# Kernel tuning notes

Hardware: AMD Instinct MI355X
Metric: run time of the kernel (lower is better)

## Reference

```python
import jax, jax.numpy as jnp
import numpy as np

SCALE = 1.0  # noise std used in the Gaussian log-pdf
HIGH = jax.lax.Precision.HIGHEST


def setup_inputs() -> dict:
    key = jax.random.key(0)
    k1, k2, k3 = jax.random.split(key, 3)
    B, N, D, T = 64, 256, 64, 4096
    data = jax.random.normal(k1, (B, N, D), dtype=jnp.float32)
    targets = jax.random.normal(k2, (B, N), dtype=jnp.float32)
    task_pool = jax.random.normal(k3, (T, D, 1), dtype=jnp.float32)
    return {"data": data, "targets": targets, "task_pool": task_pool}


def reference(data, targets, task_pool):
    # data: [B, N, D], targets: [B, N], task_pool: [T, D, 1]
    W = jnp.squeeze(task_pool).T  # [D, T]
    # Per-point, per-task Gaussian log-likelihood of targets under each task weight.
    Z = jnp.einsum('bnd,dt->bnt', data, W, precision=HIGH)  # [B, N, T]
    resid = targets[:, :, None] - Z
    logp = jax.scipy.stats.norm.logpdf(resid, loc=0.0, scale=SCALE)  # [B, N, T]
    # alpha for step i (i >= 1) is the cumulative log-lik over points 0..i-1.
    cum = jnp.cumsum(logp, axis=1)          # [B, N, T]
    alphas = cum[:, :-1]                    # [B, N-1, T], alphas[:, i-1] = alpha at step i
    post = jax.nn.softmax(alphas, axis=-1)  # posterior over tasks per step
    # MMSE weight per step: posterior-weighted average of task weights.
    w_mmse = jnp.einsum('bit,dt->bid', post, W, precision=HIGH)  # [B, N-1, D]
    preds_rest = jnp.einsum('bid,bid->bi', data[:, 1:], w_mmse)  # [B, N-1]
    # Step 0: prior mean weight (uniform average over task pool).
    pred0 = data[:, 0] @ W.mean(axis=1)  # [B]
    return jnp.concatenate([pred0[:, None], preds_rest], axis=1)  # [B, N]
```

## Files before the change

kernel.cpp:

```cpp
#include <hip/hip_runtime.h>
#include <math.h>

#define BB 64
#define NN 256
#define DD 64
#define TT 4096

#define NCH 16
#define CT (TT/NCH)
#define THREADS 512
#define WAVES 8
#define NB 16
#define NGRP (NN/NB)
#define BN (BB*NN)

#define NHL2E (-0.72134752044448170368f)

typedef __bf16 bf16x8 __attribute__((ext_vector_type(8)));
typedef float  f32x4  __attribute__((ext_vector_type(4)));

#define SHR1 0x111
#define SHR2 0x112
#define SHR4 0x114
#define SHR8 0x118

template<int C>
__device__ __forceinline__ float dppf(float x) {
  return __int_as_float(__builtin_amdgcn_update_dpp(
      0, __float_as_int(x), C, 0xf, 0xf, true));
}

__device__ __forceinline__ float bcast15(float x) {
  return __int_as_float(__builtin_amdgcn_ds_swizzle(__float_as_int(x), 0x1F0));
}

__device__ __forceinline__ unsigned short f2bf(float f) {
  unsigned int u = __float_as_uint(f);
  unsigned int r = u + 0x7FFFu + ((u >> 16) & 1u);
  return (unsigned short)(r >> 16);
}
__device__ __forceinline__ float bf2f(unsigned short h) {
  return __uint_as_float(((unsigned int)h) << 16);
}

#define GLOAD_LDS16(gp, lp_) \
  __builtin_amdgcn_global_load_lds((const __attribute__((address_space(1))) void*)(gp), \
                                   (__attribute__((address_space(3))) void*)(lp_), 16, 0, 0)

union FragU { unsigned int u[4]; bf16x8 v; };

__device__ __forceinline__ void merge8(const float2 (*sb)[16], int lane,
                                       float2* __restrict__ part, size_t obase) {
  const int col = lane & 15;
  float2 p0 = sb[0][col];
  float M = p0.x, S = 1.f, V = p0.y;
  #pragma unroll
  for (int w = 1; w < WAVES; ++w) {
    float2 pw = sb[w][col];
    float mn = fmaxf(M, pw.x);
    float ea = __builtin_amdgcn_exp2f(M - mn);
    float eb = __builtin_amdgcn_exp2f(pw.x - mn);
    S = S * ea + eb;
    V = fmaf(V, ea, pw.y * eb);
    M = mn;
  }
  if (lane < 16) {
    float2 lr;
    lr.x = M + __log2f(S);
    lr.y = V / S;
    part[obase + (size_t)col * NCH] = lr;
  }
}

__global__ __launch_bounds__(THREADS, 4)
void mmse_phase1(const float* __restrict__ data,
                 const float* __restrict__ targets,
                 const float* __restrict__ Wp,
                 float2* __restrict__ part)
{
  const int bx   = blockIdx.x;
  const int b    = bx >> 4;
  const int ch   = bx & 15;
  const int tid  = threadIdx.x;
  const int lane = tid & 63;
  const int wave = tid >> 6;

  __shared__ uint4  dbufq[2][256];
  __shared__ float  tgl[NN];
  __shared__ float2 sbuf[2][WAVES][16];

  unsigned char* dbufc = (unsigned char*)dbufq;

  bf16x8 aH[2][2], aL[2][2];
  {
    const int tb = ch * CT + wave * 32;
    #pragma unroll
    for (int tile = 0; tile < 2; ++tile) {
      #pragma unroll
      for (int s = 0; s < 2; ++s) {
        const int row = tb + tile * 16 + (lane & 15);
        const int kb  = s * 32 + (lane >> 4) * 8;
        const float* wp = Wp + (size_t)row * DD + kb;
        FragU hu, lu;
        #pragma unroll
        for (int jj = 0; jj < 4; ++jj) {
          const float f0 = wp[2 * jj], f1 = wp[2 * jj + 1];
          const unsigned short h0 = f2bf(f0), h1 = f2bf(f1);
          const unsigned short g0 = f2bf(f0 - bf2f(h0)), g1 = f2bf(f1 - bf2f(h1));
          hu.u[jj] = (unsigned int)h0 | ((unsigned int)h1 << 16);
          lu.u[jj] = (unsigned int)g0 | ((unsigned int)g1 << 16);
        }
        aH[tile][s] = hu.v; aL[tile][s] = lu.v;
      }
    }
  }

  if (wave == 0)
    GLOAD_LDS16(targets + (size_t)b * NN + lane * 4, tgl);

  const float* __restrict__ dbase = data + (size_t)b * NN * DD;
  const int sn  = tid >> 5;
  const int sk2 = tid & 31;
  const int sphys = (sn * 128 + sk2 * 4) ^ ((sn & 7) << 4);

  {
    const float2 q = *(const float2*)(dbase + (size_t)sn * DD + sk2 * 2);
    const unsigned short h0 = f2bf(q.x), h1 = f2bf(q.y);
    const unsigned short g0 = f2bf(q.x - bf2f(h0)), g1 = f2bf(q.y - bf2f(h1));
    *(unsigned int*)(dbufc + sphys)        = (unsigned int)h0 | ((unsigned int)h1 << 16);
    *(unsigned int*)(dbufc + 2048 + sphys) = (unsigned int)g0 | ((unsigned int)g1 << 16);
  }
  __syncthreads();

  float c8[8];
  #pragma unroll
  for (int i = 0; i < 8; ++i) c8[i] = 0.f;

  const size_t obase0 = (size_t)(b * NN) * NCH + ch;

  #pragma unroll 1
  for (int g = 0; g < NGRP; ++g) {
    const int buf = g & 1;
    const unsigned char* bp = dbufc + buf * 4096;
    const int ra = ((lane & 15) * 128 + (lane >> 4) * 16) ^ ((lane & 7) << 4);
    bf16x8 bh0 = *(const bf16x8*)(bp + ra);
    bf16x8 bh1 = *(const bf16x8*)(bp + (ra ^ 64));
    bf16x8 bl0 = *(const bf16x8*)(bp + 2048 + ra);
    bf16x8 bl1 = *(const bf16x8*)(bp + 2048 + (ra ^ 64));

    float2 q;
    if (g + 1 < NGRP)
      q = *(const float2*)(dbase + (size_t)((g + 1) * NB + sn) * DD + sk2 * 2);

    if (g > 0 && wave == ((g - 1) & 7))
      merge8(sbuf[(g - 1) & 1], lane, part, obase0 + (size_t)((g - 1) * NB) * NCH);

    f32x4 zz[2];
    zz[0] = (f32x4)(0.f); zz[1] = (f32x4)(0.f);
    zz[0] = __builtin_amdgcn_mfma_f32_16x16x32_bf16(aH[0][0], bh0, zz[0], 0, 0, 0);
    zz[0] = __builtin_amdgcn_mfma_f32_16x16x32_bf16(aH[0][0], bl0, zz[0], 0, 0, 0);
    zz[0] = __builtin_amdgcn_mfma_f32_16x16x32_bf16(aL[0][0], bh0, zz[0], 0, 0, 0);
    zz[0] = __builtin_amdgcn_mfma_f32_16x16x32_bf16(aH[0][1], bh1, zz[0], 0, 0, 0);
    zz[0] = __builtin_amdgcn_mfma_f32_16x16x32_bf16(aH[0][1], bl1, zz[0], 0, 0, 0);
    zz[0] = __builtin_amdgcn_mfma_f32_16x16x32_bf16(aL[0][1], bh1, zz[0], 0, 0, 0);
    zz[1] = __builtin_amdgcn_mfma_f32_16x16x32_bf16(aH[1][0], bh0, zz[1], 0, 0, 0);
    zz[1] = __builtin_amdgcn_mfma_f32_16x16x32_bf16(aH[1][0], bl0, zz[1], 0, 0, 0);
    zz[1] = __builtin_amdgcn_mfma_f32_16x16x32_bf16(aL[1][0], bh0, zz[1], 0, 0, 0);
    zz[1] = __builtin_amdgcn_mfma_f32_16x16x32_bf16(aH[1][1], bh1, zz[1], 0, 0, 0);
    zz[1] = __builtin_amdgcn_mfma_f32_16x16x32_bf16(aH[1][1], bl1, zz[1], 0, 0, 0);
    zz[1] = __builtin_amdgcn_mfma_f32_16x16x32_bf16(aL[1][1], bh1, zz[1], 0, 0, 0);

    const float tgf = tgl[g * 16 + (lane & 15)];

    float alpha[8];
    float mloc = -3.4e38f;
    #pragma unroll
    for (int tile = 0; tile < 2; ++tile) {
      #pragma unroll
      for (int r = 0; r < 4; ++r) {
        const int t8 = tile * 4 + r;
        const float z  = zz[tile][r];
        const float rr = tgf - z;
        const float lp = rr * rr * NHL2E;
        float x = lp;
        x += dppf<SHR1>(x);
        x += dppf<SHR2>(x);
        x += dppf<SHR4>(x);
        x += dppf<SHR8>(x);
        const float tot = bcast15(x);
        const float a_ = c8[t8] + (x - lp);
        alpha[t8] = a_;
        c8[t8] += tot;
        mloc = fmaxf(mloc, a_);
      }
    }
    float m = fmaxf(mloc, __shfl_xor(mloc, 16));
    m = fmaxf(m, __shfl_xor(m, 32));
    float sv = 0.f, vv = 0.f;
    #pragma unroll
    for (int tile = 0; tile < 2; ++tile) {
      #pragma unroll
      for (int r = 0; r < 4; ++r) {
        const float p = __builtin_amdgcn_exp2f(alpha[tile * 4 + r] - m);
        sv += p;
        vv = fmaf(p, zz[tile][r], vv);
      }
    }
    sv += __shfl_xor(sv, 16); sv += __shfl_xor(sv, 32);
    vv += __shfl_xor(vv, 16); vv += __shfl_xor(vv, 32);
    if (lane < 16) {
      float2 lr;
      lr.x = m + __log2f(sv);
      lr.y = vv / sv;
      sbuf[buf][wave][lane] = lr;
    }

    if (g + 1 < NGRP) {
      const unsigned short h0 = f2bf(q.x), h1 = f2bf(q.y);
      const unsigned short g0 = f2bf(q.x - bf2f(h0)), g1 = f2bf(q.y - bf2f(h1));
      unsigned char* wb = dbufc + (buf ^ 1) * 4096;
      *(unsigned int*)(wb + sphys)        = (unsigned int)h0 | ((unsigned int)h1 << 16);
      *(unsigned int*)(wb + 2048 + sphys) = (unsigned int)g0 | ((unsigned int)g1 << 16);
    }
    __syncthreads();
  }

  if (wave == ((NGRP - 1) & 7))
    merge8(sbuf[(NGRP - 1) & 1], lane, part, obase0 + (size_t)((NGRP - 1) * NB) * NCH);
}

__global__ __launch_bounds__(256)
void mmse_phase2(const float* __restrict__ part, float* __restrict__ out)
{
  const int gid  = blockIdx.x * 256 + threadIdx.x;
  const int idx  = gid >> 1;
  const int half = gid & 1;
  const float2* __restrict__ p = (const float2*)part + (size_t)idx * NCH + half * 8;
  float M = -3.4e38f, S = 0.f, V = 0.f;
  #pragma unroll
  for (int c = 0; c < 8; ++c) {
    const float2 q = p[c];
    const float mn = fmaxf(M, q.x);
    const float ea = __builtin_amdgcn_exp2f(M - mn);
    const float eb = __builtin_amdgcn_exp2f(q.x - mn);
    S = fmaf(S, ea, eb);
    V = fmaf(V, ea, q.y * eb);
    M = mn;
  }
  const float m2 = __shfl_xor(M, 1), s2 = __shfl_xor(S, 1), v2 = __shfl_xor(V, 1);
  const float mn = fmaxf(M, m2);
  const float ea = __builtin_amdgcn_exp2f(M - mn);
  const float eb = __builtin_amdgcn_exp2f(m2 - mn);
  S = fmaf(S, ea, s2 * eb);
  V = fmaf(V, ea, v2 * eb);
  if (half == 0) out[idx] = V / S;
}

extern "C" void kernel_launch(void* const* d_in, const int* in_sizes, int n_in,
                              void* d_out, int out_size, void* d_ws, size_t ws_size,
                              hipStream_t stream)
{
  const float* data      = (const float*)d_in[0];
  const float* targets   = (const float*)d_in[1];
  const float* task_pool = (const float*)d_in[2];
  float* out = (float*)d_out;

  float2* part = (float2*)d_ws;

  hipLaunchKernelGGL(mmse_phase1, dim3(BB * NCH), dim3(THREADS), 0, stream,
                     data, targets, task_pool, part);
  hipLaunchKernelGGL(mmse_phase2, dim3(2 * BN / 256), dim3(256), 0, stream,
                     (const float*)part, out);
}
```

Before: 120.3 us.

## Process 32 points per barrier step with vectorized loads and native bf16 conversion

Doubles the points per group from 16 to 32, so each loop iteration handles two 16-point halves between barriers. This halves the number of __syncthreads and merge steps. It also switches the data and weight loads to float4 and uses the hardware __bf16 conversion instead of manual bit rounding. MFMA sections are wrapped in s_setprio. The cost is a larger LDS buffer and more registers per iteration, and merge32 now uses 32 lanes.

```diff
diff --git a/kernel.cpp b/kernel.cpp
--- a/kernel.cpp
+++ b/kernel.cpp
@@ -10,12 +10,13 @@
 #define CT (TT/NCH)
 #define THREADS 512
 #define WAVES 8
-#define NB 16
+#define NB 32
 #define NGRP (NN/NB)
 #define BN (BB*NN)
 
 #define NHL2E (-0.72134752044448170368f)
 
+typedef __bf16 bf16x4 __attribute__((ext_vector_type(4)));
 typedef __bf16 bf16x8 __attribute__((ext_vector_type(8)));
 typedef float  f32x4  __attribute__((ext_vector_type(4)));
 
@@ -34,24 +35,13 @@
   return __int_as_float(__builtin_amdgcn_ds_swizzle(__float_as_int(x), 0x1F0));
 }
 
-__device__ __forceinline__ unsigned short f2bf(float f) {
-  unsigned int u = __float_as_uint(f);
-  unsigned int r = u + 0x7FFFu + ((u >> 16) & 1u);
-  return (unsigned short)(r >> 16);
-}
-__device__ __forceinline__ float bf2f(unsigned short h) {
-  return __uint_as_float(((unsigned int)h) << 16);
-}
-
 #define GLOAD_LDS16(gp, lp_) \
   __builtin_amdgcn_global_load_lds((const __attribute__((address_space(1))) void*)(gp), \
                                    (__attribute__((address_space(3))) void*)(lp_), 16, 0, 0)
 
-union FragU { unsigned int u[4]; bf16x8 v; };
-
-__device__ __forceinline__ void merge8(const float2 (*sb)[16], int lane,
-                                       float2* __restrict__ part, size_t obase) {
-  const int col = lane & 15;
+__device__ __forceinline__ void merge32(const float2 (*sb)[NB], int lane,
+                                        float2* __restrict__ part, size_t obase) {
+  const int col = lane & 31;
   float2 p0 = sb[0][col];
   float M = p0.x, S = 1.f, V = p0.y;
   #pragma unroll
@@ -64,7 +54,7 @@
     V = fmaf(V, ea, pw.y * eb);
     M = mn;
   }
-  if (lane < 16) {
+  if (lane < 32) {
     float2 lr;
     lr.x = M + __log2f(S);
     lr.y = V / S;
@@ -85,9 +75,9 @@
   const int lane = tid & 63;
   const int wave = tid >> 6;
 
-  __shared__ uint4  dbufq[2][256];
+  __shared__ uint4  dbufq[2][512];
   __shared__ float  tgl[NN];
-  __shared__ float2 sbuf[2][WAVES][16];
+  __shared__ float2 sbuf[2][WAVES][NB];
 
   unsigned char* dbufc = (unsigned char*)dbufq;
 
@@ -101,16 +91,17 @@
         const int row = tb + tile * 16 + (lane & 15);
         const int kb  = s * 32 + (lane >> 4) * 8;
         const float* wp = Wp + (size_t)row * DD + kb;
-        FragU hu, lu;
+        const float4 qa = *(const float4*)wp;
+        const float4 qb = *(const float4*)(wp + 4);
+        float f[8] = {qa.x, qa.y, qa.z, qa.w, qb.x, qb.y, qb.z, qb.w};
+        bf16x8 hv, lv;
         #pragma unroll
-        for (int jj = 0; jj < 4; ++jj) {
-          const float f0 = wp[2 * jj], f1 = wp[2 * jj + 1];
-          const unsigned short h0 = f2bf(f0), h1 = f2bf(f1);
-          const unsigned short g0 = f2bf(f0 - bf2f(h0)), g1 = f2bf(f1 - bf2f(h1));
-          hu.u[jj] = (unsigned int)h0 | ((unsigned int)h1 << 16);
-          lu.u[jj] = (unsigned int)g0 | ((unsigned int)g1 << 16);
+        for (int j = 0; j < 8; ++j) {
+          const __bf16 hj = (__bf16)f[j];
+          hv[j] = hj;
+          lv[j] = (__bf16)(f[j] - (float)hj);
         }
-        aH[tile][s] = hu.v; aL[tile][s] = lu.v;
+        aH[tile][s] = hv; aL[tile][s] = lv;
       }
     }
   }
@@ -119,16 +110,22 @@
     GLOAD_LDS16(targets + (size_t)b * NN + lane * 4, tgl);
 
   const float* __restrict__ dbase = data + (size_t)b * NN * DD;
-  const int sn  = tid >> 5;
-  const int sk2 = tid & 31;
-  const int sphys = (sn * 128 + sk2 * 4) ^ ((sn & 7) << 4);
+  const int sn  = tid >> 4;
+  const int sk8 = tid & 15;
+  const int sphys = (sn * 128 + sk8 * 8) ^ ((sn & 7) << 4);
 
   {
-    const float2 q = *(const float2*)(dbase + (size_t)sn * DD + sk2 * 2);
-    const unsigned short h0 = f2bf(q.x), h1 = f2bf(q.y);
-    const unsigned short g0 = f2bf(q.x - bf2f(h0)), g1 = f2bf(q.y - bf2f(h1));
-    *(unsigned int*)(dbufc + sphys)        = (unsigned int)h0 | ((unsigned int)h1 << 16);
-    *(unsigned int*)(dbufc + 2048 + sphys) = (unsigned int)g0 | ((unsigned int)g1 << 16);
+    const float4 q = *(const float4*)(dbase + (size_t)sn * DD + sk8 * 4);
+    float f[4] = {q.x, q.y, q.z, q.w};
+    bf16x4 hv, lv;
+    #pragma unroll
+    for (int j = 0; j < 4; ++j) {
+      const __bf16 hj = (__bf16)f[j];
+      hv[j] = hj;
+      lv[j] = (__bf16)(f[j] - (float)hj);
+    }
+    *(bf16x4*)(dbufc + sphys)        = hv;
+    *(bf16x4*)(dbufc + 4096 + sphys) = lv;
   }
   __syncthreads();
 
@@ -137,96 +134,109 @@
   for (int i = 0; i < 8; ++i) c8[i] = 0.f;
 
   const size_t obase0 = (size_t)(b * NN) * NCH + ch;
+  const int ra = ((lane & 15) * 128 + (lane >> 4) * 16) ^ ((lane & 7) << 4);
 
   #pragma unroll 1
   for (int g = 0; g < NGRP; ++g) {
     const int buf = g & 1;
-    const unsigned char* bp = dbufc + buf * 4096;
-    const int ra = ((lane & 15) * 128 + (lane >> 4) * 16) ^ ((lane & 7) << 4);
-    bf16x8 bh0 = *(const bf16x8*)(bp + ra);
-    bf16x8 bh1 = *(const bf16x8*)(bp + (ra ^ 64));
-    bf16x8 bl0 = *(const bf16x8*)(bp + 2048 + ra);
-    bf16x8 bl1 = *(const bf16x8*)(bp + 2048 + (ra ^ 64));
-
-    float2 q;
+    const unsigned char* bp = dbufc + buf * 8192;
+
+    float4 q;
     if (g + 1 < NGRP)
-      q = *(const float2*)(dbase + (size_t)((g + 1) * NB + sn) * DD + sk2 * 2);
+      q = *(const float4*)(dbase + (size_t)((g + 1) * NB + sn) * DD + sk8 * 4);
 
     if (g > 0 && wave == ((g - 1) & 7))
-      merge8(sbuf[(g - 1) & 1], lane, part, obase0 + (size_t)((g - 1) * NB) * NCH);
-
-    f32x4 zz[2];
-    zz[0] = (f32x4)(0.f); zz[1] = (f32x4)(0.f);
-    zz[0] = __builtin_amdgcn_mfma_f32_16x16x32_bf16(aH[0][0], bh0, zz[0], 0, 0, 0);
-    zz[0] = __builtin_amdgcn_mfma_f32_16x16x32_bf16(aH[0][0], bl0, zz[0], 0, 0, 0);
-    zz[0] = __builtin_amdgcn_mfma_f32_16x16x32_bf16(aL[0][0], bh0, zz[0], 0, 0, 0);
-    zz[0] = __builtin_amdgcn_mfma_f32_16x16x32_bf16(aH[0][1], bh1, zz[0], 0, 0, 0);
-    zz[0] = __builtin_amdgcn_mfma_f32_16x16x32_bf16(aH[0][1], bl1, zz[0], 0, 0, 0);
-    zz[0] = __builtin_amdgcn_mfma_f32_16x16x32_bf16(aL[0][1], bh1, zz[0], 0, 0, 0);
-    zz[1] = __builtin_amdgcn_mfma_f32_16x16x32_bf16(aH[1][0], bh0, zz[1], 0, 0, 0);
-    zz[1] = __builtin_amdgcn_mfma_f32_16x16x32_bf16(aH[1][0], bl0, zz[1], 0, 0, 0);
-    zz[1] = __builtin_amdgcn_mfma_f32_16x16x32_bf16(aL[1][0], bh0, zz[1], 0, 0, 0);
-    zz[1] = __builtin_amdgcn_mfma_f32_16x16x32_bf16(aH[1][1], bh1, zz[1], 0, 0, 0);
-    zz[1] = __builtin_amdgcn_mfma_f32_16x16x32_bf16(aH[1][1], bl1, zz[1], 0, 0, 0);
-    zz[1] = __builtin_amdgcn_mfma_f32_16x16x32_bf16(aL[1][1], bh1, zz[1], 0, 0, 0);
-
-    const float tgf = tgl[g * 16 + (lane & 15)];
-
-    float alpha[8];
-    float mloc = -3.4e38f;
+      merge32(sbuf[(g - 1) & 1], lane, part, obase0 + (size_t)((g - 1) * NB) * NCH);
+
     #pragma unroll
-    for (int tile = 0; tile < 2; ++tile) {
-      #pragma unroll
-      for (int r = 0; r < 4; ++r) {
-        const int t8 = tile * 4 + r;
-        const float z  = zz[tile][r];
-        const float rr = tgf - z;
-        const float lp = rr * rr * NHL2E;
-        float x = lp;
-        x += dppf<SHR1>(x);
-        x += dppf<SHR2>(x);
-        x += dppf<SHR4>(x);
-        x += dppf<SHR8>(x);
-        const float tot = bcast15(x);
-        const float a_ = c8[t8] + (x - lp);
-        alpha[t8] = a_;
-        c8[t8] += tot;
-        mloc = fmaxf(mloc, a_);
-      }
-    }
-    float m = fmaxf(mloc, __shfl_xor(mloc, 16));
-    m = fmaxf(m, __shfl_xor(m, 32));
-    float sv = 0.f, vv = 0.f;
-    #pragma unroll
-    for (int tile = 0; tile < 2; ++tile) {
-      #pragma unroll
-      for (int r = 0; r < 4; ++r) {
-        const float p = __builtin_amdgcn_exp2f(alpha[tile * 4 + r] - m);
-        sv += p;
-        vv = fmaf(p, zz[tile][r], vv);
-      }
-    }
-    sv += __shfl_xor(sv, 16); sv += __shfl_xor(sv, 32);
-    vv += __shfl_xor(vv, 16); vv += __shfl_xor(vv, 32);
-    if (lane < 16) {
-      float2 lr;
-      lr.x = m + __log2f(sv);
-      lr.y = vv / sv;
-      sbuf[buf][wave][lane] = lr;
+    for (int h = 0; h < 2; ++h) {
+      const unsigned char* hp = bp + h * 2048;
+      bf16x8 bh0 = *(const bf16x8*)(hp + ra);
+      bf16x8 bh1 = *(const bf16x8*)(hp + (ra ^ 64));
+      bf16x8 bl0 = *(const bf16x8*)(hp + 4096 + ra);
+      bf16x8 bl1 = *(const bf16x8*)(hp + 4096 + (ra ^ 64));
+
+      f32x4 zz[2];
+      zz[0] = (f32x4)(0.f); zz[1] = (f32x4)(0.f);
+      __builtin_amdgcn_s_setprio(1);
+      zz[0] = __builtin_amdgcn_mfma_f32_16x16x32_bf16(aH[0][0], bh0, zz[0], 0, 0, 0);
+      zz[0] = __builtin_amdgcn_mfma_f32_16x16x32_bf16(aH[0][0], bl0, zz[0], 0, 0, 0);
+      zz[0] = __builtin_amdgcn_mfma_f32_16x16x32_bf16(aL[0][0], bh0, zz[0], 0, 0, 0);
+      zz[0] = __builtin_amdgcn_mfma_f32_16x16x32_bf16(aH[0][1], bh1, zz[0], 0, 0, 0);
+      zz[0] = __builtin_amdgcn_mfma_f32_16x16x32_bf16(aH[0][1], bl1, zz[0], 0, 0, 0);
+      zz[0] = __builtin_amdgcn_mfma_f32_16x16x32_bf16(aL[0][1], bh1, zz[0], 0, 0, 0);
+      zz[1] = __builtin_amdgcn_mfma_f32_16x16x32_bf16(aH[1][0], bh0, zz[1], 0, 0, 0);
+      zz[1] = __builtin_amdgcn_mfma_f32_16x16x32_bf16(aH[1][0], bl0, zz[1], 0, 0, 0);
+      zz[1] = __builtin_amdgcn_mfma_f32_16x16x32_bf16(aL[1][0], bh0, zz[1], 0, 0, 0);
+      zz[1] = __builtin_amdgcn_mfma_f32_16x16x32_bf16(aH[1][1], bh1, zz[1], 0, 0, 0);
+      zz[1] = __builtin_amdgcn_mfma_f32_16x16x32_bf16(aH[1][1], bl1, zz[1], 0, 0, 0);
+      zz[1] = __builtin_amdgcn_mfma_f32_16x16x32_bf16(aL[1][1], bh1, zz[1], 0, 0, 0);
+      __builtin_amdgcn_s_setprio(0);
+
+      const float tgf = tgl[g * NB + h * 16 + (lane & 15)];
+
+      float alpha[8];
+      float mloc = -3.4e38f;
+      #pragma unroll
+      for (int tile = 0; tile < 2; ++tile) {
+        #pragma unroll
+        for (int r = 0; r < 4; ++r) {
+          const int t8 = tile * 4 + r;
+          const float z  = zz[tile][r];
+          const float rr = tgf - z;
+          const float lp = rr * rr * NHL2E;
+          float x = lp;
+          x += dppf<SHR1>(x);
+          x += dppf<SHR2>(x);
+          x += dppf<SHR4>(x);
+          x += dppf<SHR8>(x);
+          const float tot = bcast15(x);
+          const float a_ = c8[t8] + (x - lp);
+          alpha[t8] = a_;
+          c8[t8] += tot;
+          mloc = fmaxf(mloc, a_);
+        }
+      }
+      float m = fmaxf(mloc, __shfl_xor(mloc, 16));
+      m = fmaxf(m, __shfl_xor(m, 32));
+      float sv = 0.f, vv = 0.f;
+      #pragma unroll
+      for (int tile = 0; tile < 2; ++tile) {
+        #pragma unroll
+        for (int r = 0; r < 4; ++r) {
+          const float p = __builtin_amdgcn_exp2f(alpha[tile * 4 + r] - m);
+          sv += p;
+          vv = fmaf(p, zz[tile][r], vv);
+        }
+      }
+      sv += __shfl_xor(sv, 16); sv += __shfl_xor(sv, 32);
+      vv += __shfl_xor(vv, 16); vv += __shfl_xor(vv, 32);
+      if (lane < 16) {
+        float2 lr;
+        lr.x = m + __log2f(sv);
+        lr.y = vv / sv;
+        sbuf[buf][wave][h * 16 + lane] = lr;
+      }
     }
 
     if (g + 1 < NGRP) {
-      const unsigned short h0 = f2bf(q.x), h1 = f2bf(q.y);
-      const unsigned short g0 = f2bf(q.x - bf2f(h0)), g1 = f2bf(q.y - bf2f(h1));
-      unsigned char* wb = dbufc + (buf ^ 1) * 4096;
-      *(unsigned int*)(wb + sphys)        = (unsigned int)h0 | ((unsigned int)h1 << 16);
-      *(unsigned int*)(wb + 2048 + sphys) = (unsigned int)g0 | ((unsigned int)g1 << 16);
+      float f[4] = {q.x, q.y, q.z, q.w};
+      bf16x4 hv, lv;
+      #pragma unroll
+      for (int j = 0; j < 4; ++j) {
+        const __bf16 hj = (__bf16)f[j];
+        hv[j] = hj;
+        lv[j] = (__bf16)(f[j] - (float)hj);
+      }
+      unsigned char* wb = dbufc + (buf ^ 1) * 8192;
+      *(bf16x4*)(wb + sphys)        = hv;
+      *(bf16x4*)(wb + 4096 + sphys) = lv;
     }
     __syncthreads();
   }
 
   if (wave == ((NGRP - 1) & 7))
-    merge8(sbuf[(NGRP - 1) & 1], lane, part, obase0 + (size_t)((NGRP - 1) * NB) * NCH);
+    merge32(sbuf[(NGRP - 1) & 1], lane, part, obase0 + (size_t)((NGRP - 1) * NB) * NCH);
 }
 
 __global__ __launch_bounds__(256)
```

New measurement: 112.3 us. -6.6%, faster.
